# Kernel tuning notes

Measured on AMD Instinct MI355X. Metric: run time of the kernel, lower is better.

Reference implementation:

```python
import jax, jax.numpy as jnp
import numpy as np

D = 1024
H = 16
HD = D // H
SCALE = HD ** -0.5
LN_EPS = 1e-5


def _ln(x, g, b):
    m = x.mean(-1, keepdims=True)
    v = ((x - m) ** 2).mean(-1, keepdims=True)
    return (x - m) / jnp.sqrt(v + LN_EPS) * g + b


def _heads(x):
    B, S, _ = x.shape
    return x.reshape(B, S, H, HD).transpose(0, 2, 1, 3)  # [B,H,S,hd]


def setup_inputs() -> dict:
    key = jax.random.key(0)
    ks = jax.random.split(key, 32)
    it = iter(ks)

    def w():
        return jax.random.normal(next(it), (D, D), dtype=jnp.float32) * 0.02

    inp = {
        'q_text': jax.random.normal(next(it), (4, 512, D), dtype=jnp.float32),
        'q_image': jax.random.normal(next(it), (4, 576, D), dtype=jnp.float32),
        'k_text': jax.random.normal(next(it), (4, 512, D), dtype=jnp.float32),
        'k_image': jax.random.normal(next(it), (4, 576, D), dtype=jnp.float32),
        'Wq_text': w(), 'bq_text': jnp.zeros((D,), jnp.float32),
        'Wk_text': w(), 'bk_text': jnp.zeros((D,), jnp.float32),
        'Wv_text': w(), 'bv_text': jnp.zeros((D,), jnp.float32),
        'Wq_image': w(), 'bq_image': jnp.zeros((D,), jnp.float32),
        'Wk_image': w(), 'bk_image': jnp.zeros((D,), jnp.float32),
        'Wv_image': w(), 'bv_image': jnp.zeros((D,), jnp.float32),
        'ln_g_text': jnp.ones((D,), jnp.float32), 'ln_b_text': jnp.zeros((D,), jnp.float32),
        'ln_g_image': jnp.ones((D,), jnp.float32), 'ln_b_image': jnp.zeros((D,), jnp.float32),
        'Wo': w(), 'bo': jnp.zeros((D,), jnp.float32),
    }
    return inp


def reference(q_text, q_image, k_text, k_image,
              Wq_text, bq_text, Wk_text, bk_text, Wv_text, bv_text,
              Wq_image, bq_image, Wk_image, bk_image, Wv_image, bv_image,
              ln_g_text, ln_b_text, ln_g_image, ln_b_image, Wo, bo):
    # Normalize KV inputs per modality, project, split heads, concat along seq.
    kt = _ln(k_text, ln_g_text, ln_b_text)
    ki = _ln(k_image, ln_g_image, ln_b_image)
    K = jnp.concatenate([_heads(kt @ Wk_text.T + bk_text),
                         _heads(ki @ Wk_image.T + bk_image)], axis=2)  # [B,H,Skv,hd]
    # NOTE: torch module projects V from the `keys` tensors (values dict unused)
    V = jnp.concatenate([_heads(kt @ Wv_text.T + bv_text),
                         _heads(ki @ Wv_image.T + bv_image)], axis=2)

    def attend(q, g, b, Wq, bq):
        qn = _ln(q, g, b)
        Q = _heads(qn @ Wq.T + bq) * SCALE  # [B,H,Sq,hd]
        scores = jnp.einsum('bhqd,bhkd->bhqk', Q, K)
        w = jax.nn.softmax(scores.astype(jnp.float32), axis=-1).astype(q.dtype)
        o = jnp.einsum('bhqk,bhkd->bhqd', w, V)
        B, Sq = q.shape[0], q.shape[1]
        o = o.transpose(0, 2, 1, 3).reshape(B, Sq, D)
        return o @ Wo.T + bo, w

    out_t, w_t = attend(q_text, ln_g_text, ln_b_text, Wq_text, bq_text)
    out_i, w_i = attend(q_image, ln_g_image, ln_b_image, Wq_image, bq_image)
    return out_t, out_i, w_t, w_i
```

## Files before the change

kernel.cpp:

```cpp
#include <hip/hip_runtime.h>
#include <math.h>

#define DMODEL 1024
#define SKV 1088
#define SCALE 0.125f

typedef __attribute__((ext_vector_type(8))) short short8;
typedef __attribute__((ext_vector_type(4))) float floatx4;
typedef unsigned short ush;

__device__ __forceinline__ ush bf16_rne(float f) {
  unsigned u = __float_as_uint(f);
  u = (u + 0x7FFFu + ((u >> 16) & 1u)) >> 16;
  return (ush)u;
}
__device__ __forceinline__ float bf16_f32(ush h) {
  return __uint_as_float(((unsigned)h) << 16);
}

__global__ __launch_bounds__(256) void ln_split(const float* __restrict__ x,
                                                const float* __restrict__ g,
                                                const float* __restrict__ bta,
                                                ush* __restrict__ yh,
                                                ush* __restrict__ yl) {
  int row = blockIdx.x;
  const float4* xr = (const float4*)(x + (size_t)row * DMODEL);
  float4 v = xr[threadIdx.x];
  float s = v.x + v.y + v.z + v.w;
  float s2 = v.x * v.x + v.y * v.y + v.z * v.z + v.w * v.w;
  for (int off = 32; off > 0; off >>= 1) {
    s += __shfl_down(s, off, 64);
    s2 += __shfl_down(s2, off, 64);
  }
  __shared__ float ls[4], ls2[4];
  int wid = threadIdx.x >> 6;
  if ((threadIdx.x & 63) == 0) { ls[wid] = s; ls2[wid] = s2; }
  __syncthreads();
  float tot = ls[0] + ls[1] + ls[2] + ls[3];
  float tot2 = ls2[0] + ls2[1] + ls2[2] + ls2[3];
  float mean = tot * (1.0f / DMODEL);
  float var = tot2 * (1.0f / DMODEL) - mean * mean;
  float rstd = rsqrtf(var + 1e-5f);
  float4 gv = ((const float4*)g)[threadIdx.x];
  float4 bv = ((const float4*)bta)[threadIdx.x];
  float4 o;
  o.x = (v.x - mean) * rstd * gv.x + bv.x;
  o.y = (v.y - mean) * rstd * gv.y + bv.y;
  o.z = (v.z - mean) * rstd * gv.z + bv.z;
  o.w = (v.w - mean) * rstd * gv.w + bv.w;
  ushort4 hv, lv;
  hv.x = bf16_rne(o.x); lv.x = bf16_rne(o.x - bf16_f32(hv.x));
  hv.y = bf16_rne(o.y); lv.y = bf16_rne(o.y - bf16_f32(hv.y));
  hv.z = bf16_rne(o.z); lv.z = bf16_rne(o.z - bf16_f32(hv.z));
  hv.w = bf16_rne(o.w); lv.w = bf16_rne(o.w - bf16_f32(hv.w));
  ((ushort4*)(yh + (size_t)row * DMODEL))[threadIdx.x] = hv;
  ((ushort4*)(yl + (size_t)row * DMODEL))[threadIdx.x] = lv;
}

struct ConvJob { const float* src; ush* h; ush* l; int n4; };
struct ConvJobs { ConvJob j[4]; };

__global__ __launch_bounds__(256) void conv_split(ConvJobs jobs) {
  ConvJob jb = jobs.j[blockIdx.y];
  int i = blockIdx.x * 256 + threadIdx.x;
  if (i >= jb.n4) return;
  float4 v = ((const float4*)jb.src)[i];
  ushort4 hv, lv;
  hv.x = bf16_rne(v.x); lv.x = bf16_rne(v.x - bf16_f32(hv.x));
  hv.y = bf16_rne(v.y); lv.y = bf16_rne(v.y - bf16_f32(hv.y));
  hv.z = bf16_rne(v.z); lv.z = bf16_rne(v.z - bf16_f32(hv.z));
  hv.w = bf16_rne(v.w); lv.w = bf16_rne(v.w - bf16_f32(hv.w));
  ((ushort4*)jb.h)[i] = hv;
  ((ushort4*)jb.l)[i] = lv;
}

struct GemmSJob {
  const ush *Ah, *Al, *Wh, *Wl;
  const float* bias;
  float* C;
  ush* Cb;
  int M, Sin, Sout, seq_off;
  float scale;
};
struct GemmSJobs { GemmSJob j[4]; };

__device__ __forceinline__ int lds_slot(int m, int kc) {
  return m * 32 + ((kc ^ ((m >> 2) & 3)) << 3);
}

__global__ __launch_bounds__(256) void gemm_split(GemmSJobs jobs) {
  GemmSJob jb = jobs.j[blockIdx.z];
  const int m0 = blockIdx.y * 128;
  if (m0 >= jb.M) return;
  const int n0 = blockIdx.x * 128;

  __shared__ __align__(16) ush sAh[128 * 32];
  __shared__ __align__(16) ush sAl[128 * 32];
  __shared__ __align__(16) ush sWh[128 * 32];
  __shared__ __align__(16) ush sWl[128 * 32];

  const int tid = threadIdx.x;
  const int lane = tid & 63;
  const int wv = tid >> 6;
  const int wm = (wv & 1) * 64;
  const int wn = (wv >> 1) * 64;

  const int mS = tid >> 2;
  const int kcS = tid & 3;
  const int ls0 = lds_slot(mS, kcS);
  const int ls1 = lds_slot(mS + 64, kcS);
  const size_t aOff0 = (size_t)(m0 + mS) * DMODEL + kcS * 8;
  const size_t aOff1 = (size_t)(m0 + mS + 64) * DMODEL + kcS * 8;
  const size_t wOff0 = (size_t)(n0 + mS) * DMODEL + kcS * 8;
  const size_t wOff1 = (size_t)(n0 + mS + 64) * DMODEL + kcS * 8;

  const int fr = lane & 15, fc = lane >> 4;
  int offA[4], offB[4];
#pragma unroll
  for (int t = 0; t < 4; ++t) {
    offA[t] = lds_slot(wm + t * 16 + fr, fc);
    offB[t] = lds_slot(wn + t * 16 + fr, fc);
  }

  floatx4 acc[4][4];
#pragma unroll
  for (int mt = 0; mt < 4; ++mt)
#pragma unroll
    for (int nt = 0; nt < 4; ++nt) acc[mt][nt] = (floatx4){0.f, 0.f, 0.f, 0.f};

  uint4 rAh0 = *(const uint4*)(jb.Ah + aOff0);
  uint4 rAh1 = *(const uint4*)(jb.Ah + aOff1);
  uint4 rAl0 = *(const uint4*)(jb.Al + aOff0);
  uint4 rAl1 = *(const uint4*)(jb.Al + aOff1);
  uint4 rWh0 = *(const uint4*)(jb.Wh + wOff0);
  uint4 rWh1 = *(const uint4*)(jb.Wh + wOff1);
  uint4 rWl0 = *(const uint4*)(jb.Wl + wOff0);
  uint4 rWl1 = *(const uint4*)(jb.Wl + wOff1);

  for (int k0 = 0; k0 < DMODEL; k0 += 32) {
    __syncthreads();
    *(uint4*)(sAh + ls0) = rAh0;
    *(uint4*)(sAh + ls1) = rAh1;
    *(uint4*)(sAl + ls0) = rAl0;
    *(uint4*)(sAl + ls1) = rAl1;
    *(uint4*)(sWh + ls0) = rWh0;
    *(uint4*)(sWh + ls1) = rWh1;
    *(uint4*)(sWl + ls0) = rWl0;
    *(uint4*)(sWl + ls1) = rWl1;
    __syncthreads();
    if (k0 + 32 < DMODEL) {
      const int ko = k0 + 32;
      rAh0 = *(const uint4*)(jb.Ah + aOff0 + ko);
      rAh1 = *(const uint4*)(jb.Ah + aOff1 + ko);
      rAl0 = *(const uint4*)(jb.Al + aOff0 + ko);
      rAl1 = *(const uint4*)(jb.Al + aOff1 + ko);
      rWh0 = *(const uint4*)(jb.Wh + wOff0 + ko);
      rWh1 = *(const uint4*)(jb.Wh + wOff1 + ko);
      rWl0 = *(const uint4*)(jb.Wl + wOff0 + ko);
      rWl1 = *(const uint4*)(jb.Wl + wOff1 + ko);
    }
    short8 ah[4], al[4];
#pragma unroll
    for (int t = 0; t < 4; ++t) {
      ah[t] = *(const short8*)(sAh + offA[t]);
      al[t] = *(const short8*)(sAl + offA[t]);
    }
#pragma unroll
    for (int nt = 0; nt < 4; ++nt) {
      short8 bh = *(const short8*)(sWh + offB[nt]);
      short8 bl = *(const short8*)(sWl + offB[nt]);
#pragma unroll
      for (int mt = 0; mt < 4; ++mt) {
        acc[mt][nt] = __builtin_amdgcn_mfma_f32_16x16x32_bf16(ah[mt], bh, acc[mt][nt], 0, 0, 0);
        acc[mt][nt] = __builtin_amdgcn_mfma_f32_16x16x32_bf16(ah[mt], bl, acc[mt][nt], 0, 0, 0);
        acc[mt][nt] = __builtin_amdgcn_mfma_f32_16x16x32_bf16(al[mt], bh, acc[mt][nt], 0, 0, 0);
      }
    }
  }

  float bias_v[4];
#pragma unroll
  for (int nt = 0; nt < 4; ++nt) bias_v[nt] = jb.bias[n0 + wn + nt * 16 + fr];
  if (jb.Cb) {
#pragma unroll
    for (int mt = 0; mt < 4; ++mt) {
#pragma unroll
      for (int r = 0; r < 4; ++r) {
        int rowA = m0 + wm + mt * 16 + fc * 4 + r;
        int rowOut = (rowA / jb.Sin) * jb.Sout + jb.seq_off + (rowA % jb.Sin);
        ush* crow = jb.Cb + (size_t)rowOut * DMODEL + n0 + wn + fr;
#pragma unroll
        for (int nt = 0; nt < 4; ++nt)
          crow[nt * 16] = bf16_rne((acc[mt][nt][r] + bias_v[nt]) * jb.scale);
      }
    }
  } else {
#pragma unroll
    for (int mt = 0; mt < 4; ++mt) {
#pragma unroll
      for (int r = 0; r < 4; ++r) {
        int rowA = m0 + wm + mt * 16 + fc * 4 + r;
        int rowOut = (rowA / jb.Sin) * jb.Sout + jb.seq_off + (rowA % jb.Sin);
        float* crow = jb.C + (size_t)rowOut * DMODEL + n0 + wn + fr;
#pragma unroll
        for (int nt = 0; nt < 4; ++nt)
          crow[nt * 16] = (acc[mt][nt][r] + bias_v[nt]) * jb.scale;
      }
    }
  }
}

__global__ __launch_bounds__(256) void vtrans(const float* __restrict__ Vc, ush* __restrict__ Vt) {
  int k0 = blockIdx.x * 64;
  int bh = blockIdx.y;
  int b = bh >> 4, h = bh & 15;
  __shared__ ush T[64][72];
  int t = threadIdx.x;
  int c4 = (t & 15) * 4;
  int r = t >> 4;
#pragma unroll
  for (int i = 0; i < 4; ++i) {
    int kr = r + i * 16;
    float4 v = *(const float4*)(Vc + (size_t)(b * SKV + k0 + kr) * DMODEL + h * 64 + c4);
    T[c4 + 0][kr] = bf16_rne(v.x);
    T[c4 + 1][kr] = bf16_rne(v.y);
    T[c4 + 2][kr] = bf16_rne(v.z);
    T[c4 + 3][kr] = bf16_rne(v.w);
  }
  __syncthreads();
#pragma unroll
  for (int i = 0; i < 4; ++i) {
    int dr = r + i * 16;
    ushort4 o;
    o.x = T[dr][c4 + 0]; o.y = T[dr][c4 + 1]; o.z = T[dr][c4 + 2]; o.w = T[dr][c4 + 3];
    *(ushort4*)(Vt + ((size_t)bh * 64 + dr) * SKV + k0 + c4) = o;
  }
}

__global__ __launch_bounds__(256) void attn_mfma(
    const ush* __restrict__ Qt, const ush* __restrict__ Qi,
    const ush* __restrict__ Kbf, const ush* __restrict__ Vtp,
    float* __restrict__ Wt, float* __restrict__ Wi,
    ush* __restrict__ OtH, ush* __restrict__ OtL,
    ush* __restrict__ OiH, ush* __restrict__ OiL) {
  const int mod = blockIdx.z;
  const int Sq = mod ? 576 : 512;
  const int q0 = blockIdx.x * 32;
  if (q0 >= Sq) return;
  const int bh = blockIdx.y;
  const int b = bh >> 4, h = bh & 15;
  const ush* Q = mod ? Qi : Qt;
  float* Wout = mod ? Wi : Wt;
  ush* OH = mod ? OiH : OtH;
  ush* OL = mod ? OiL : OtL;

  const int tid = threadIdx.x;
  const int lane = tid & 63;
  const int wv = tid >> 6;
  const int qs = (wv & 1) * 16;
  const int half = wv >> 1;
  const int fr = lane & 15;
  const int fc = lane >> 4;

  __shared__ ush Psh[32][80];
  __shared__ float sm[2][2][16], sl[2][2][16];

  const ush* qrow = Q + (size_t)(b * Sq + q0 + qs + fr) * DMODEL + h * 64 + fc * 8;
  short8 qa0 = *(const short8*)qrow;
  short8 qa1 = *(const short8*)(qrow + 32);

  const ush* Kbase = Kbf + (size_t)b * SKV * DMODEL + h * 64 + fc * 8;
  const ush* Vbase = Vtp + (size_t)bh * 64 * SKV;

  float m[4], l[4];
#pragma unroll
  for (int r = 0; r < 4; ++r) { m[r] = -1e30f; l[r] = 0.f; }

  for (int k0 = 0; k0 < SKV; k0 += 64) {
    const ush* kr0 = Kbase + (size_t)(k0 + half * 32 + fr) * DMODEL;
    const ush* kr1 = kr0 + 16 * DMODEL;
    short8 b00 = *(const short8*)kr0;
    short8 b01 = *(const short8*)(kr0 + 32);
    short8 b10 = *(const short8*)kr1;
    short8 b11 = *(const short8*)(kr1 + 32);
    floatx4 s0 = (floatx4){0.f, 0.f, 0.f, 0.f};
    floatx4 s1 = (floatx4){0.f, 0.f, 0.f, 0.f};
    s0 = __builtin_amdgcn_mfma_f32_16x16x32_bf16(qa0, b00, s0, 0, 0, 0);
    s0 = __builtin_amdgcn_mfma_f32_16x16x32_bf16(qa1, b01, s0, 0, 0, 0);
    s1 = __builtin_amdgcn_mfma_f32_16x16x32_bf16(qa0, b10, s1, 0, 0, 0);
    s1 = __builtin_amdgcn_mfma_f32_16x16x32_bf16(qa1, b11, s1, 0, 0, 0);
#pragma unroll
    for (int r = 0; r < 4; ++r) {
      float mn = fmaxf(m[r], fmaxf(s0[r], s1[r]));
      l[r] = l[r] * __expf(m[r] - mn) + __expf(s0[r] - mn) + __expf(s1[r] - mn);
      m[r] = mn;
    }
  }
#pragma unroll
  for (int off = 1; off <= 8; off <<= 1) {
#pragma unroll
    for (int r = 0; r < 4; ++r) {
      float mo = __shfl_xor(m[r], off, 64);
      float lo = __shfl_xor(l[r], off, 64);
      float mn = fmaxf(m[r], mo);
      l[r] = l[r] * __expf(m[r] - mn) + lo * __expf(mo - mn);
      m[r] = mn;
    }
  }
  if (fr == 0) {
#pragma unroll
    for (int r = 0; r < 4; ++r) {
      sm[half][wv & 1][fc * 4 + r] = m[r];
      sl[half][wv & 1][fc * 4 + r] = l[r];
    }
  }
  __syncthreads();
  float mf[4], rl[4];
#pragma unroll
  for (int r = 0; r < 4; ++r) {
    int row = fc * 4 + r;
    float ma = sm[0][wv & 1][row], mb = sm[1][wv & 1][row];
    float la = sl[0][wv & 1][row], lb = sl[1][wv & 1][row];
    float mn = fmaxf(ma, mb);
    float lt = la * __expf(ma - mn) + lb * __expf(mb - mn);
    mf[r] = mn;
    rl[r] = 1.0f / lt;
  }

  floatx4 oacc0 = (floatx4){0.f, 0.f, 0.f, 0.f};
  floatx4 oacc1 = (floatx4){0.f, 0.f, 0.f, 0.f};

  for (int k0 = 0; k0 < SKV; k0 += 64) {
    const ush* kr0 = Kbase + (size_t)(k0 + half * 32 + fr) * DMODEL;
    const ush* kr1 = kr0 + 16 * DMODEL;
    short8 b00 = *(const short8*)kr0;
    short8 b01 = *(const short8*)(kr0 + 32);
    short8 b10 = *(const short8*)kr1;
    short8 b11 = *(const short8*)(kr1 + 32);
    floatx4 s0 = (floatx4){0.f, 0.f, 0.f, 0.f};
    floatx4 s1 = (floatx4){0.f, 0.f, 0.f, 0.f};
    s0 = __builtin_amdgcn_mfma_f32_16x16x32_bf16(qa0, b00, s0, 0, 0, 0);
    s0 = __builtin_amdgcn_mfma_f32_16x16x32_bf16(qa1, b01, s0, 0, 0, 0);
    s1 = __builtin_amdgcn_mfma_f32_16x16x32_bf16(qa0, b10, s1, 0, 0, 0);
    s1 = __builtin_amdgcn_mfma_f32_16x16x32_bf16(qa1, b11, s1, 0, 0, 0);
#pragma unroll
    for (int r = 0; r < 4; ++r) {
      float w0 = __expf(s0[r] - mf[r]) * rl[r];
      float w1 = __expf(s1[r] - mf[r]) * rl[r];
      int q = q0 + qs + fc * 4 + r;
      float* wr = Wout + ((size_t)bh * Sq + q) * SKV + k0 + half * 32 + fr;
      wr[0] = w0;
      wr[16] = w1;
      Psh[qs + fc * 4 + r][half * 32 + fr] = bf16_rne(w0);
      Psh[qs + fc * 4 + r][half * 32 + 16 + fr] = bf16_rne(w1);
    }
    __syncthreads();
    short8 pa0 = *(const short8*)&Psh[qs + fr][fc * 8];
    short8 pa1 = *(const short8*)&Psh[qs + fr][32 + fc * 8];
    const ush* v0 = Vbase + (size_t)(half * 32 + fr) * SKV + k0 + fc * 8;
    const ush* v1 = v0 + (size_t)16 * SKV;
    short8 vb00 = *(const short8*)v0;
    short8 vb01 = *(const short8*)(v0 + 32);
    short8 vb10 = *(const short8*)v1;
    short8 vb11 = *(const short8*)(v1 + 32);
    oacc0 = __builtin_amdgcn_mfma_f32_16x16x32_bf16(pa0, vb00, oacc0, 0, 0, 0);
    oacc0 = __builtin_amdgcn_mfma_f32_16x16x32_bf16(pa1, vb01, oacc0, 0, 0, 0);
    oacc1 = __builtin_amdgcn_mfma_f32_16x16x32_bf16(pa0, vb10, oacc1, 0, 0, 0);
    oacc1 = __builtin_amdgcn_mfma_f32_16x16x32_bf16(pa1, vb11, oacc1, 0, 0, 0);
    __syncthreads();
  }

#pragma unroll
  for (int r = 0; r < 4; ++r) {
    int q = q0 + qs + fc * 4 + r;
    size_t orow = (size_t)(b * Sq + q) * DMODEL + h * 64;
    float o0 = oacc0[r], o1 = oacc1[r];
    ush h0 = bf16_rne(o0);
    ush h1 = bf16_rne(o1);
    OH[orow + half * 32 + fr] = h0;
    OL[orow + half * 32 + fr] = bf16_rne(o0 - bf16_f32(h0));
    OH[orow + half * 32 + 16 + fr] = h1;
    OL[orow + half * 32 + 16 + fr] = bf16_rne(o1 - bf16_f32(h1));
  }
}

extern "C" void kernel_launch(void* const* d_in, const int* in_sizes, int n_in,
                              void* d_out, int out_size, void* d_ws, size_t ws_size,
                              hipStream_t stream) {
  const float* q_text = (const float*)d_in[0];
  const float* q_image = (const float*)d_in[1];
  const float* k_text = (const float*)d_in[2];
  const float* k_image = (const float*)d_in[3];
  const float* Wq_t = (const float*)d_in[4];
  const float* bq_t = (const float*)d_in[5];
  const float* Wk_t = (const float*)d_in[6];
  const float* bk_t = (const float*)d_in[7];
  const float* Wv_t = (const float*)d_in[8];
  const float* bv_t = (const float*)d_in[9];
  const float* Wq_i = (const float*)d_in[10];
  const float* bq_i = (const float*)d_in[11];
  const float* Wk_i = (const float*)d_in[12];
  const float* bk_i = (const float*)d_in[13];
  const float* Wv_i = (const float*)d_in[14];
  const float* bv_i = (const float*)d_in[15];
  const float* g_t = (const float*)d_in[16];
  const float* b_t = (const float*)d_in[17];
  const float* g_i = (const float*)d_in[18];
  const float* b_i = (const float*)d_in[19];
  const float* Wo = (const float*)d_in[20];
  const float* bo = (const float*)d_in[21];

  float* out = (float*)d_out;
  float* out_t = out;
  float* out_i = out + 2097152;
  float* w_t = out + 4456448;
  float* w_i = out + 40108032;

  char* W = (char*)d_ws;
  ush* Kbf = (ush*)(W + 0);
  ush* Qt_bf = (ush*)(W + 8912896);
  ush* Qi_bf = (ush*)(W + 13107200);
  float* Vc = (float*)(W + 17825792);
  ush* Vt = (ush*)(W + 35651584);
  char* R0 = W + 44564480;

  ush* knt_h = (ush*)(R0 + 0);
  ush* knt_l = (ush*)(R0 + 4194304);
  ush* kni_h = (ush*)(R0 + 8388608);
  ush* kni_l = (ush*)(R0 + 13107200);
  ush* wkt_h = (ush*)(R0 + 17825792);
  ush* wkt_l = (ush*)(R0 + 19922944);
  ush* wki_h = (ush*)(R0 + 22020096);
  ush* wki_l = (ush*)(R0 + 24117248);
  ush* wvt_h = (ush*)(R0 + 26214400);
  ush* wvt_l = (ush*)(R0 + 28311552);
  ush* wvi_h = (ush*)(R0 + 30408704);
  ush* wvi_l = (ush*)(R0 + 32505856);
  ush* qnt_h = (ush*)(R0 + 0);
  ush* qnt_l = (ush*)(R0 + 4194304);
  ush* qni_h = (ush*)(R0 + 8388608);
  ush* qni_l = (ush*)(R0 + 13107200);
  ush* wqt_h = (ush*)(R0 + 17825792);
  ush* wqt_l = (ush*)(R0 + 19922944);
  ush* wqi_h = (ush*)(R0 + 22020096);
  ush* wqi_l = (ush*)(R0 + 24117248);
  ush* ot_h = (ush*)(R0 + 0);
  ush* ot_l = (ush*)(R0 + 4194304);
  ush* oi_h = (ush*)(R0 + 8388608);
  ush* oi_l = (ush*)(R0 + 13107200);
  ush* wo_h = (ush*)(R0 + 17825792);
  ush* wo_l = (ush*)(R0 + 19922944);

  ln_split<<<2048, 256, 0, stream>>>(k_text, g_t, b_t, knt_h, knt_l);
  ln_split<<<2304, 256, 0, stream>>>(k_image, g_i, b_i, kni_h, kni_l);

  ConvJobs cw;
  cw.j[0] = {Wk_t, wkt_h, wkt_l, 262144};
  cw.j[1] = {Wk_i, wki_h, wki_l, 262144};
  cw.j[2] = {Wv_t, wvt_h, wvt_l, 262144};
  cw.j[3] = {Wv_i, wvi_h, wvi_l, 262144};
  conv_split<<<dim3(1024, 4), 256, 0, stream>>>(cw);

  GemmSJobs kv;
  kv.j[0] = {knt_h, knt_l, wkt_h, wkt_l, bk_t, nullptr, Kbf, 2048, 512, SKV, 0, 1.0f};
  kv.j[1] = {kni_h, kni_l, wki_h, wki_l, bk_i, nullptr, Kbf, 2304, 576, SKV, 512, 1.0f};
  kv.j[2] = {knt_h, knt_l, wvt_h, wvt_l, bv_t, Vc, nullptr, 2048, 512, SKV, 0, 1.0f};
  kv.j[3] = {kni_h, kni_l, wvi_h, wvi_l, bv_i, Vc, nullptr, 2304, 576, SKV, 512, 1.0f};
  gemm_split<<<dim3(8, 18, 4), 256, 0, stream>>>(kv);

  vtrans<<<dim3(17, 64), 256, 0, stream>>>(Vc, Vt);

  ln_split<<<2048, 256, 0, stream>>>(q_text, g_t, b_t, qnt_h, qnt_l);
  ln_split<<<2304, 256, 0, stream>>>(q_image, g_i, b_i, qni_h, qni_l);

  ConvJobs cq;
  cq.j[0] = {Wq_t, wqt_h, wqt_l, 262144};
  cq.j[1] = {Wq_i, wqi_h, wqi_l, 262144};
  cq.j[2] = cq.j[0];
  cq.j[3] = cq.j[0];
  conv_split<<<dim3(1024, 2), 256, 0, stream>>>(cq);

  GemmSJobs qj;
  qj.j[0] = {qnt_h, qnt_l, wqt_h, wqt_l, bq_t, nullptr, Qt_bf, 2048, 512, 512, 0, SCALE};
  qj.j[1] = {qni_h, qni_l, wqi_h, wqi_l, bq_i, nullptr, Qi_bf, 2304, 576, 576, 0, SCALE};
  qj.j[2] = qj.j[0];
  qj.j[3] = qj.j[0];
  gemm_split<<<dim3(8, 18, 2), 256, 0, stream>>>(qj);

  attn_mfma<<<dim3(18, 64, 2), 256, 0, stream>>>(Qt_bf, Qi_bf, Kbf, Vt,
                                                 w_t, w_i, ot_h, ot_l, oi_h, oi_l);

  ConvJobs cwo;
  cwo.j[0] = {Wo, wo_h, wo_l, 262144};
  cwo.j[1] = cwo.j[0];
  cwo.j[2] = cwo.j[0];
  cwo.j[3] = cwo.j[0];
  conv_split<<<dim3(1024, 1), 256, 0, stream>>>(cwo);

  GemmSJobs oj;
  oj.j[0] = {ot_h, ot_l, wo_h, wo_l, bo, out_t, nullptr, 2048, 512, 512, 0, 1.0f};
  oj.j[1] = {oi_h, oi_l, wo_h, wo_l, bo, out_i, nullptr, 2304, 576, 576, 0, 1.0f};
  oj.j[2] = oj.j[0];
  oj.j[3] = oj.j[0];
  gemm_split<<<dim3(8, 18, 2), 256, 0, stream>>>(oj);
}
```

Baseline: 774.8 us.

## Batch LN/convert/projection launches, use direct-to-LDS GEMM loads, restructure attention with LDS tiles

Merges the four layernorm launches into one, the K/V/Q weight conversions into one, and the K/V/Q projection GEMMs into a single six-job launch. V is now written as bf16 instead of fp32, which halves the transpose traffic. The GEMM stages tiles through global_load_lds when available, but it drops the register prefetch and so loses load/compute overlap. Attention now uses 64-query blocks that share K/V tiles in swizzled LDS across four waves, trading extra barriers for less redundant global traffic.

```diff
diff --git a/kernel.cpp b/kernel.cpp
--- a/kernel.cpp
+++ b/kernel.cpp
@@ -18,13 +18,26 @@
   return __uint_as_float(((unsigned)h) << 16);
 }
 
-__global__ __launch_bounds__(256) void ln_split(const float* __restrict__ x,
-                                                const float* __restrict__ g,
-                                                const float* __restrict__ bta,
-                                                ush* __restrict__ yh,
-                                                ush* __restrict__ yl) {
+#if __has_builtin(__builtin_amdgcn_global_load_lds)
+#define HAS_GLL 1
+__device__ __forceinline__ void gll16(const ush* g, ush* l) {
+  __builtin_amdgcn_global_load_lds(
+      (const __attribute__((address_space(1))) unsigned int*)g,
+      (__attribute__((address_space(3))) unsigned int*)(unsigned int)(size_t)l,
+      16, 0, 0);
+}
+#else
+#define HAS_GLL 0
+#endif
+
+struct LnJob { const float* x; const float* g; const float* b; ush* yh; ush* yl; int rows; };
+struct LnJobs { LnJob j[4]; };
+
+__global__ __launch_bounds__(256) void ln_all(LnJobs jobs) {
+  LnJob jb = jobs.j[blockIdx.y];
   int row = blockIdx.x;
-  const float4* xr = (const float4*)(x + (size_t)row * DMODEL);
+  if (row >= jb.rows) return;
+  const float4* xr = (const float4*)(jb.x + (size_t)row * DMODEL);
   float4 v = xr[threadIdx.x];
   float s = v.x + v.y + v.z + v.w;
   float s2 = v.x * v.x + v.y * v.y + v.z * v.z + v.w * v.w;
@@ -41,8 +54,8 @@
   float mean = tot * (1.0f / DMODEL);
   float var = tot2 * (1.0f / DMODEL) - mean * mean;
   float rstd = rsqrtf(var + 1e-5f);
-  float4 gv = ((const float4*)g)[threadIdx.x];
-  float4 bv = ((const float4*)bta)[threadIdx.x];
+  float4 gv = ((const float4*)jb.g)[threadIdx.x];
+  float4 bv = ((const float4*)jb.b)[threadIdx.x];
   float4 o;
   o.x = (v.x - mean) * rstd * gv.x + bv.x;
   o.y = (v.y - mean) * rstd * gv.y + bv.y;
@@ -53,12 +66,12 @@
   hv.y = bf16_rne(o.y); lv.y = bf16_rne(o.y - bf16_f32(hv.y));
   hv.z = bf16_rne(o.z); lv.z = bf16_rne(o.z - bf16_f32(hv.z));
   hv.w = bf16_rne(o.w); lv.w = bf16_rne(o.w - bf16_f32(hv.w));
-  ((ushort4*)(yh + (size_t)row * DMODEL))[threadIdx.x] = hv;
-  ((ushort4*)(yl + (size_t)row * DMODEL))[threadIdx.x] = lv;
+  ((ushort4*)(jb.yh + (size_t)row * DMODEL))[threadIdx.x] = hv;
+  ((ushort4*)(jb.yl + (size_t)row * DMODEL))[threadIdx.x] = lv;
 }
 
 struct ConvJob { const float* src; ush* h; ush* l; int n4; };
-struct ConvJobs { ConvJob j[4]; };
+struct ConvJobs { ConvJob j[6]; };
 
 __global__ __launch_bounds__(256) void conv_split(ConvJobs jobs) {
   ConvJob jb = jobs.j[blockIdx.y];
@@ -82,7 +95,7 @@
   int M, Sin, Sout, seq_off;
   float scale;
 };
-struct GemmSJobs { GemmSJob j[4]; };
+struct GemmSJobs { GemmSJob j[6]; };
 
 __device__ __forceinline__ int lds_slot(int m, int kc) {
   return m * 32 + ((kc ^ ((m >> 2) & 3)) << 3);
@@ -94,10 +107,10 @@
   if (m0 >= jb.M) return;
   const int n0 = blockIdx.x * 128;
 
-  __shared__ __align__(16) ush sAh[128 * 32];
-  __shared__ __align__(16) ush sAl[128 * 32];
-  __shared__ __align__(16) ush sWh[128 * 32];
-  __shared__ __align__(16) ush sWl[128 * 32];
+  __shared__ __align__(16) ush sAh[4096];
+  __shared__ __align__(16) ush sAl[4096];
+  __shared__ __align__(16) ush sWh[4096];
+  __shared__ __align__(16) ush sWl[4096];
 
   const int tid = threadIdx.x;
   const int lane = tid & 63;
@@ -105,14 +118,14 @@
   const int wm = (wv & 1) * 64;
   const int wn = (wv >> 1) * 64;
 
-  const int mS = tid >> 2;
-  const int kcS = tid & 3;
-  const int ls0 = lds_slot(mS, kcS);
-  const int ls1 = lds_slot(mS + 64, kcS);
-  const size_t aOff0 = (size_t)(m0 + mS) * DMODEL + kcS * 8;
-  const size_t aOff1 = (size_t)(m0 + mS + 64) * DMODEL + kcS * 8;
-  const size_t wOff0 = (size_t)(n0 + mS) * DMODEL + kcS * 8;
-  const size_t wOff1 = (size_t)(n0 + mS + 64) * DMODEL + kcS * 8;
+  const int rowS = tid >> 2;
+  const int kcS = (tid & 3) ^ ((rowS >> 2) & 3);
+  const size_t aOff0 = (size_t)(m0 + rowS) * DMODEL + kcS * 8;
+  const size_t aOff1 = aOff0 + (size_t)64 * DMODEL;
+  const size_t wOff0 = (size_t)(n0 + rowS) * DMODEL + kcS * 8;
+  const size_t wOff1 = wOff0 + (size_t)64 * DMODEL;
+  const int lq0 = tid * 8;
+  const int lq1 = 2048 + tid * 8;
 
   const int fr = lane & 15, fc = lane >> 4;
   int offA[4], offB[4];
@@ -128,37 +141,34 @@
 #pragma unroll
     for (int nt = 0; nt < 4; ++nt) acc[mt][nt] = (floatx4){0.f, 0.f, 0.f, 0.f};
 
-  uint4 rAh0 = *(const uint4*)(jb.Ah + aOff0);
-  uint4 rAh1 = *(const uint4*)(jb.Ah + aOff1);
-  uint4 rAl0 = *(const uint4*)(jb.Al + aOff0);
-  uint4 rAl1 = *(const uint4*)(jb.Al + aOff1);
-  uint4 rWh0 = *(const uint4*)(jb.Wh + wOff0);
-  uint4 rWh1 = *(const uint4*)(jb.Wh + wOff1);
-  uint4 rWl0 = *(const uint4*)(jb.Wl + wOff0);
-  uint4 rWl1 = *(const uint4*)(jb.Wl + wOff1);
-
   for (int k0 = 0; k0 < DMODEL; k0 += 32) {
     __syncthreads();
-    *(uint4*)(sAh + ls0) = rAh0;
-    *(uint4*)(sAh + ls1) = rAh1;
-    *(uint4*)(sAl + ls0) = rAl0;
-    *(uint4*)(sAl + ls1) = rAl1;
-    *(uint4*)(sWh + ls0) = rWh0;
-    *(uint4*)(sWh + ls1) = rWh1;
-    *(uint4*)(sWl + ls0) = rWl0;
-    *(uint4*)(sWl + ls1) = rWl1;
+#if HAS_GLL
+    gll16(jb.Ah + aOff0 + k0, sAh + lq0);
+    gll16(jb.Ah + aOff1 + k0, sAh + lq1);
+    gll16(jb.Al + aOff0 + k0, sAl + lq0);
+    gll16(jb.Al + aOff1 + k0, sAl + lq1);
+    gll16(jb.Wh + wOff0 + k0, sWh + lq0);
+    gll16(jb.Wh + wOff1 + k0, sWh + lq1);
+    gll16(jb.Wl + wOff0 + k0, sWl + lq0);
+    gll16(jb.Wl + wOff1 + k0, sWl + lq1);
+#else
+    {
+      uint4 a0 = *(const uint4*)(jb.Ah + aOff0 + k0);
+      uint4 a1 = *(const uint4*)(jb.Ah + aOff1 + k0);
+      uint4 b0 = *(const uint4*)(jb.Al + aOff0 + k0);
+      uint4 b1 = *(const uint4*)(jb.Al + aOff1 + k0);
+      uint4 c0 = *(const uint4*)(jb.Wh + wOff0 + k0);
+      uint4 c1 = *(const uint4*)(jb.Wh + wOff1 + k0);
+      uint4 d0 = *(const uint4*)(jb.Wl + wOff0 + k0);
+      uint4 d1 = *(const uint4*)(jb.Wl + wOff1 + k0);
+      *(uint4*)(sAh + lq0) = a0; *(uint4*)(sAh + lq1) = a1;
+      *(uint4*)(sAl + lq0) = b0; *(uint4*)(sAl + lq1) = b1;
+      *(uint4*)(sWh + lq0) = c0; *(uint4*)(sWh + lq1) = c1;
+      *(uint4*)(sWl + lq0) = d0; *(uint4*)(sWl + lq1) = d1;
+    }
+#endif
     __syncthreads();
-    if (k0 + 32 < DMODEL) {
-      const int ko = k0 + 32;
-      rAh0 = *(const uint4*)(jb.Ah + aOff0 + ko);
-      rAh1 = *(const uint4*)(jb.Ah + aOff1 + ko);
-      rAl0 = *(const uint4*)(jb.Al + aOff0 + ko);
-      rAl1 = *(const uint4*)(jb.Al + aOff1 + ko);
-      rWh0 = *(const uint4*)(jb.Wh + wOff0 + ko);
-      rWh1 = *(const uint4*)(jb.Wh + wOff1 + ko);
-      rWl0 = *(const uint4*)(jb.Wl + wOff0 + ko);
-      rWl1 = *(const uint4*)(jb.Wl + wOff1 + ko);
-    }
     short8 ah[4], al[4];
 #pragma unroll
     for (int t = 0; t < 4; ++t) {
@@ -210,7 +220,7 @@
   }
 }
 
-__global__ __launch_bounds__(256) void vtrans(const float* __restrict__ Vc, ush* __restrict__ Vt) {
+__global__ __launch_bounds__(256) void vtrans(const ush* __restrict__ Vbf, ush* __restrict__ Vt) {
   int k0 = blockIdx.x * 64;
   int bh = blockIdx.y;
   int b = bh >> 4, h = bh & 15;
@@ -221,11 +231,11 @@
 #pragma unroll
   for (int i = 0; i < 4; ++i) {
     int kr = r + i * 16;
-    float4 v = *(const float4*)(Vc + (size_t)(b * SKV + k0 + kr) * DMODEL + h * 64 + c4);
-    T[c4 + 0][kr] = bf16_rne(v.x);
-    T[c4 + 1][kr] = bf16_rne(v.y);
-    T[c4 + 2][kr] = bf16_rne(v.z);
-    T[c4 + 3][kr] = bf16_rne(v.w);
+    ushort4 v = *(const ushort4*)(Vbf + (size_t)(b * SKV + k0 + kr) * DMODEL + h * 64 + c4);
+    T[c4 + 0][kr] = v.x;
+    T[c4 + 1][kr] = v.y;
+    T[c4 + 2][kr] = v.z;
+    T[c4 + 3][kr] = v.w;
   }
   __syncthreads();
 #pragma unroll
@@ -238,61 +248,86 @@
 }
 
 __global__ __launch_bounds__(256) void attn_mfma(
-    const ush* __restrict__ Qt, const ush* __restrict__ Qi,
+    const ush* __restrict__ Qtb, const ush* __restrict__ Qib,
     const ush* __restrict__ Kbf, const ush* __restrict__ Vtp,
     float* __restrict__ Wt, float* __restrict__ Wi,
     ush* __restrict__ OtH, ush* __restrict__ OtL,
     ush* __restrict__ OiH, ush* __restrict__ OiL) {
   const int mod = blockIdx.z;
   const int Sq = mod ? 576 : 512;
-  const int q0 = blockIdx.x * 32;
+  const int q0 = blockIdx.x * 64;
   if (q0 >= Sq) return;
   const int bh = blockIdx.y;
   const int b = bh >> 4, h = bh & 15;
-  const ush* Q = mod ? Qi : Qt;
+  const ush* Q = mod ? Qib : Qtb;
   float* Wout = mod ? Wi : Wt;
   ush* OH = mod ? OiH : OtH;
   ush* OL = mod ? OiL : OtL;
 
+  __shared__ __align__(16) ush sK[64 * 64];
+  __shared__ __align__(16) ush sV[64 * 64];
+  __shared__ __align__(16) ush sP[4][16 * 64];
+
   const int tid = threadIdx.x;
   const int lane = tid & 63;
   const int wv = tid >> 6;
-  const int qs = (wv & 1) * 16;
-  const int half = wv >> 1;
   const int fr = lane & 15;
   const int fc = lane >> 4;
 
-  __shared__ ush Psh[32][80];
-  __shared__ float sm[2][2][16], sl[2][2][16];
-
-  const ush* qrow = Q + (size_t)(b * Sq + q0 + qs + fr) * DMODEL + h * 64 + fc * 8;
+  const int srow = tid >> 2;
+  const int sch = (tid & 3) * 2;
+  const int ssl = sch ^ (srow & 7);
+  ush* skw0 = sK + srow * 64 + ssl * 8;
+  ush* skw1 = sK + srow * 64 + (ssl ^ 1) * 8;
+  ush* svw0 = sV + srow * 64 + ssl * 8;
+  ush* svw1 = sV + srow * 64 + (ssl ^ 1) * 8;
+  const ush* Kg = Kbf + (size_t)(b * SKV + srow) * DMODEL + h * 64 + sch * 8;
+  const ush* Vg = Vtp + ((size_t)bh * 64 + srow) * SKV + sch * 8;
+
+  const ush* qrow = Q + (size_t)(b * Sq + q0 + wv * 16 + fr) * DMODEL + h * 64 + fc * 8;
   short8 qa0 = *(const short8*)qrow;
   short8 qa1 = *(const short8*)(qrow + 32);
 
-  const ush* Kbase = Kbf + (size_t)b * SKV * DMODEL + h * 64 + fc * 8;
-  const ush* Vbase = Vtp + (size_t)bh * 64 * SKV;
+  const int sw = fr & 7;
+  int kOffL[4], kOffH[4];
+#pragma unroll
+  for (int j = 0; j < 4; ++j) {
+    int base = (j * 16 + fr) * 64;
+    kOffL[j] = base + (fc ^ sw) * 8;
+    kOffH[j] = base + ((fc + 4) ^ sw) * 8;
+  }
+  const int pOffL = fr * 64 + (fc ^ sw) * 8;
+  const int pOffH = fr * 64 + ((fc + 4) ^ sw) * 8;
 
   float m[4], l[4];
 #pragma unroll
-  for (int r = 0; r < 4; ++r) { m[r] = -1e30f; l[r] = 0.f; }
-
-  for (int k0 = 0; k0 < SKV; k0 += 64) {
-    const ush* kr0 = Kbase + (size_t)(k0 + half * 32 + fr) * DMODEL;
-    const ush* kr1 = kr0 + 16 * DMODEL;
-    short8 b00 = *(const short8*)kr0;
-    short8 b01 = *(const short8*)(kr0 + 32);
-    short8 b10 = *(const short8*)kr1;
-    short8 b11 = *(const short8*)(kr1 + 32);
-    floatx4 s0 = (floatx4){0.f, 0.f, 0.f, 0.f};
-    floatx4 s1 = (floatx4){0.f, 0.f, 0.f, 0.f};
-    s0 = __builtin_amdgcn_mfma_f32_16x16x32_bf16(qa0, b00, s0, 0, 0, 0);
-    s0 = __builtin_amdgcn_mfma_f32_16x16x32_bf16(qa1, b01, s0, 0, 0, 0);
-    s1 = __builtin_amdgcn_mfma_f32_16x16x32_bf16(qa0, b10, s1, 0, 0, 0);
-    s1 = __builtin_amdgcn_mfma_f32_16x16x32_bf16(qa1, b11, s1, 0, 0, 0);
+  for (int r = 0; r < 4; ++r) { m[r] = -3e38f; l[r] = 0.f; }
+
+  for (int kt = 0; kt < 17; ++kt) {
+    __syncthreads();
+    {
+      const ush* kp = Kg + (size_t)(kt * 64) * DMODEL;
+      uint4 x = *(const uint4*)kp;
+      uint4 y = *(const uint4*)(kp + 8);
+      *(uint4*)skw0 = x;
+      *(uint4*)skw1 = y;
+    }
+    __syncthreads();
+    floatx4 s[4];
+#pragma unroll
+    for (int j = 0; j < 4; ++j) {
+      short8 b0 = *(const short8*)(sK + kOffL[j]);
+      short8 b1 = *(const short8*)(sK + kOffH[j]);
+      floatx4 z = (floatx4){0.f, 0.f, 0.f, 0.f};
+      z = __builtin_amdgcn_mfma_f32_16x16x32_bf16(qa0, b0, z, 0, 0, 0);
+      s[j] = __builtin_amdgcn_mfma_f32_16x16x32_bf16(qa1, b1, z, 0, 0, 0);
+    }
 #pragma unroll
     for (int r = 0; r < 4; ++r) {
-      float mn = fmaxf(m[r], fmaxf(s0[r], s1[r]));
-      l[r] = l[r] * __expf(m[r] - mn) + __expf(s0[r] - mn) + __expf(s1[r] - mn);
+      float mx = fmaxf(fmaxf(s[0][r], s[1][r]), fmaxf(s[2][r], s[3][r]));
+      float mn = fmaxf(m[r], mx);
+      l[r] = l[r] * __expf(m[r] - mn) + __expf(s[0][r] - mn) + __expf(s[1][r] - mn) +
+             __expf(s[2][r] - mn) + __expf(s[3][r] - mn);
       m[r] = mn;
     }
   }
@@ -307,80 +342,74 @@
       m[r] = mn;
     }
   }
-  if (fr == 0) {
+  float rl[4];
+#pragma unroll
+  for (int r = 0; r < 4; ++r) rl[r] = 1.0f / l[r];
+
+  floatx4 oacc[4];
+#pragma unroll
+  for (int j = 0; j < 4; ++j) oacc[j] = (floatx4){0.f, 0.f, 0.f, 0.f};
+
+  float* wbase = Wout + ((size_t)bh * Sq + q0 + wv * 16) * SKV;
+
+  for (int kt = 0; kt < 17; ++kt) {
+    const int k0 = kt * 64;
+    __syncthreads();
+    {
+      const ush* kp = Kg + (size_t)k0 * DMODEL;
+      uint4 x = *(const uint4*)kp;
+      uint4 y = *(const uint4*)(kp + 8);
+      const ush* vp = Vg + k0;
+      uint4 vx = *(const uint4*)vp;
+      uint4 vy = *(const uint4*)(vp + 8);
+      *(uint4*)skw0 = x;
+      *(uint4*)skw1 = y;
+      *(uint4*)svw0 = vx;
+      *(uint4*)svw1 = vy;
+    }
+    __syncthreads();
+    floatx4 s[4];
+#pragma unroll
+    for (int j = 0; j < 4; ++j) {
+      short8 b0 = *(const short8*)(sK + kOffL[j]);
+      short8 b1 = *(const short8*)(sK + kOffH[j]);
+      floatx4 z = (floatx4){0.f, 0.f, 0.f, 0.f};
+      z = __builtin_amdgcn_mfma_f32_16x16x32_bf16(qa0, b0, z, 0, 0, 0);
+      s[j] = __builtin_amdgcn_mfma_f32_16x16x32_bf16(qa1, b1, s[j] = z, 0, 0, 0);
+    }
+#pragma unroll
+    for (int j = 0; j < 4; ++j) {
+#pragma unroll
+      for (int r = 0; r < 4; ++r) {
+        float w = __expf(s[j][r] - m[r]) * rl[r];
+        wbase[(size_t)(fc * 4 + r) * SKV + k0 + j * 16 + fr] = w;
+        int row = fc * 4 + r;
+        int chunk = j * 2 + (fr >> 3);
+        sP[wv][row * 64 + ((chunk ^ (row & 7)) * 8) + (fr & 7)] = bf16_rne(w);
+      }
+    }
+    short8 pa0 = *(const short8*)(sP[wv] + pOffL);
+    short8 pa1 = *(const short8*)(sP[wv] + pOffH);
+#pragma unroll
+    for (int j = 0; j < 4; ++j) {
+      short8 v0 = *(const short8*)(sV + kOffL[j]);
+      short8 v1 = *(const short8*)(sV + kOffH[j]);
+      oacc[j] = __builtin_amdgcn_mfma_f32_16x16x32_bf16(pa0, v0, oacc[j], 0, 0, 0);
+      oacc[j] = __builtin_amdgcn_mfma_f32_16x16x32_bf16(pa1, v1, oacc[j], 0, 0, 0);
+    }
+  }
+
+#pragma unroll
+  for (int j = 0; j < 4; ++j) {
 #pragma unroll
     for (int r = 0; r < 4; ++r) {
-      sm[half][wv & 1][fc * 4 + r] = m[r];
-      sl[half][wv & 1][fc * 4 + r] = l[r];
-    }
-  }
-  __syncthreads();
-  float mf[4], rl[4];
-#pragma unroll
-  for (int r = 0; r < 4; ++r) {
-    int row = fc * 4 + r;
-    float ma = sm[0][wv & 1][row], mb = sm[1][wv & 1][row];
-    float la = sl[0][wv & 1][row], lb = sl[1][wv & 1][row];
-    float mn = fmaxf(ma, mb);
-    float lt = la * __expf(ma - mn) + lb * __expf(mb - mn);
-    mf[r] = mn;
-    rl[r] = 1.0f / lt;
-  }
-
-  floatx4 oacc0 = (floatx4){0.f, 0.f, 0.f, 0.f};
-  floatx4 oacc1 = (floatx4){0.f, 0.f, 0.f, 0.f};
-
-  for (int k0 = 0; k0 < SKV; k0 += 64) {
-    const ush* kr0 = Kbase + (size_t)(k0 + half * 32 + fr) * DMODEL;
-    const ush* kr1 = kr0 + 16 * DMODEL;
-    short8 b00 = *(const short8*)kr0;
-    short8 b01 = *(const short8*)(kr0 + 32);
-    short8 b10 = *(const short8*)kr1;
-    short8 b11 = *(const short8*)(kr1 + 32);
-    floatx4 s0 = (floatx4){0.f, 0.f, 0.f, 0.f};
-    floatx4 s1 = (floatx4){0.f, 0.f, 0.f, 0.f};
-    s0 = __builtin_amdgcn_mfma_f32_16x16x32_bf16(qa0, b00, s0, 0, 0, 0);
-    s0 = __builtin_amdgcn_mfma_f32_16x16x32_bf16(qa1, b01, s0, 0, 0, 0);
-    s1 = __builtin_amdgcn_mfma_f32_16x16x32_bf16(qa0, b10, s1, 0, 0, 0);
-    s1 = __builtin_amdgcn_mfma_f32_16x16x32_bf16(qa1, b11, s1, 0, 0, 0);
-#pragma unroll
-    for (int r = 0; r < 4; ++r) {
-      float w0 = __expf(s0[r] - mf[r]) * rl[r];
-      float w1 = __expf(s1[r] - mf[r]) * rl[r];
-      int q = q0 + qs + fc * 4 + r;
-      float* wr = Wout + ((size_t)bh * Sq + q) * SKV + k0 + half * 32 + fr;
-      wr[0] = w0;
-      wr[16] = w1;
-      Psh[qs + fc * 4 + r][half * 32 + fr] = bf16_rne(w0);
-      Psh[qs + fc * 4 + r][half * 32 + 16 + fr] = bf16_rne(w1);
-    }
-    __syncthreads();
-    short8 pa0 = *(const short8*)&Psh[qs + fr][fc * 8];
-    short8 pa1 = *(const short8*)&Psh[qs + fr][32 + fc * 8];
-    const ush* v0 = Vbase + (size_t)(half * 32 + fr) * SKV + k0 + fc * 8;
-    const ush* v1 = v0 + (size_t)16 * SKV;
-    short8 vb00 = *(const short8*)v0;
-    short8 vb01 = *(const short8*)(v0 + 32);
-    short8 vb10 = *(const short8*)v1;
-    short8 vb11 = *(const short8*)(v1 + 32);
-    oacc0 = __builtin_amdgcn_mfma_f32_16x16x32_bf16(pa0, vb00, oacc0, 0, 0, 0);
-    oacc0 = __builtin_amdgcn_mfma_f32_16x16x32_bf16(pa1, vb01, oacc0, 0, 0, 0);
-    oacc1 = __builtin_amdgcn_mfma_f32_16x16x32_bf16(pa0, vb10, oacc1, 0, 0, 0);
-    oacc1 = __builtin_amdgcn_mfma_f32_16x16x32_bf16(pa1, vb11, oacc1, 0, 0, 0);
-    __syncthreads();
-  }
-
-#pragma unroll
-  for (int r = 0; r < 4; ++r) {
-    int q = q0 + qs + fc * 4 + r;
-    size_t orow = (size_t)(b * Sq + q) * DMODEL + h * 64;
-    float o0 = oacc0[r], o1 = oacc1[r];
-    ush h0 = bf16_rne(o0);
-    ush h1 = bf16_rne(o1);
-    OH[orow + half * 32 + fr] = h0;
-    OL[orow + half * 32 + fr] = bf16_rne(o0 - bf16_f32(h0));
-    OH[orow + half * 32 + 16 + fr] = h1;
-    OL[orow + half * 32 + 16 + fr] = bf16_rne(o1 - bf16_f32(h1));
+      int q = q0 + wv * 16 + fc * 4 + r;
+      size_t oidx = (size_t)(b * Sq + q) * DMODEL + h * 64 + j * 16 + fr;
+      float o = oacc[j][r];
+      ush hh = bf16_rne(o);
+      OH[oidx] = hh;
+      OL[oidx] = bf16_rne(o - bf16_f32(hh));
+    }
   }
 }
 
@@ -418,89 +447,76 @@
 
   char* W = (char*)d_ws;
   ush* Kbf = (ush*)(W + 0);
-  ush* Qt_bf = (ush*)(W + 8912896);
-  ush* Qi_bf = (ush*)(W + 13107200);
-  float* Vc = (float*)(W + 17825792);
-  ush* Vt = (ush*)(W + 35651584);
-  char* R0 = W + 44564480;
-
-  ush* knt_h = (ush*)(R0 + 0);
-  ush* knt_l = (ush*)(R0 + 4194304);
-  ush* kni_h = (ush*)(R0 + 8388608);
-  ush* kni_l = (ush*)(R0 + 13107200);
-  ush* wkt_h = (ush*)(R0 + 17825792);
-  ush* wkt_l = (ush*)(R0 + 19922944);
-  ush* wki_h = (ush*)(R0 + 22020096);
-  ush* wki_l = (ush*)(R0 + 24117248);
-  ush* wvt_h = (ush*)(R0 + 26214400);
-  ush* wvt_l = (ush*)(R0 + 28311552);
-  ush* wvi_h = (ush*)(R0 + 30408704);
-  ush* wvi_l = (ush*)(R0 + 32505856);
-  ush* qnt_h = (ush*)(R0 + 0);
-  ush* qnt_l = (ush*)(R0 + 4194304);
-  ush* qni_h = (ush*)(R0 + 8388608);
-  ush* qni_l = (ush*)(R0 + 13107200);
-  ush* wqt_h = (ush*)(R0 + 17825792);
-  ush* wqt_l = (ush*)(R0 + 19922944);
-  ush* wqi_h = (ush*)(R0 + 22020096);
-  ush* wqi_l = (ush*)(R0 + 24117248);
-  ush* ot_h = (ush*)(R0 + 0);
-  ush* ot_l = (ush*)(R0 + 4194304);
-  ush* oi_h = (ush*)(R0 + 8388608);
-  ush* oi_l = (ush*)(R0 + 13107200);
-  ush* wo_h = (ush*)(R0 + 17825792);
-  ush* wo_l = (ush*)(R0 + 19922944);
-
-  ln_split<<<2048, 256, 0, stream>>>(k_text, g_t, b_t, knt_h, knt_l);
-  ln_split<<<2304, 256, 0, stream>>>(k_image, g_i, b_i, kni_h, kni_l);
+  ush* Vbf = (ush*)(W + 8912896);
+  ush* Qt_bf = (ush*)(W + 17825792);
+  ush* Qi_bf = (ush*)(W + 22020096);
+  ush* knt_h = (ush*)(W + 26738688);
+  ush* knt_l = (ush*)(W + 30932992);
+  ush* kni_h = (ush*)(W + 35127296);
+  ush* kni_l = (ush*)(W + 39845888);
+  ush* qnt_h = (ush*)(W + 44564480);
+  ush* qnt_l = (ush*)(W + 48758784);
+  ush* qni_h = (ush*)(W + 52953088);
+  ush* qni_l = (ush*)(W + 57671680);
+  ush* wkt_h = (ush*)(W + 62390272);
+  ush* wkt_l = (ush*)(W + 64487424);
+  ush* wki_h = (ush*)(W + 66584576);
+  ush* wki_l = (ush*)(W + 68681728);
+  ush* wvt_h = (ush*)(W + 70778880);
+  ush* wvt_l = (ush*)(W + 72876032);
+  ush* wvi_h = (ush*)(W + 74973184);
+  ush* wvi_l = (ush*)(W + 77070336);
+  ush* wqt_h = (ush*)(W + 79167488);
+  ush* wqt_l = (ush*)(W + 81264640);
+  ush* wqi_h = (ush*)(W + 83361792);
+  ush* wqi_l = (ush*)(W + 85458944);
+  ush* Vt = (ush*)(W + 44564480);
+  ush* wo_h = (ush*)(W + 53477376);
+  ush* wo_l = (ush*)(W + 55574528);
+  ush* ot_h = knt_h;
+  ush* ot_l = knt_l;
+  ush* oi_h = kni_h;
+  ush* oi_l = kni_l;
+
+  LnJobs lj;
+  lj.j[0] = {k_text, g_t, b_t, knt_h, knt_l, 2048};
+  lj.j[1] = {k_image, g_i, b_i, kni_h, kni_l, 2304};
+  lj.j[2] = {q_text, g_t, b_t, qnt_h, qnt_l, 2048};
+  lj.j[3] = {q_image, g_i, b_i, qni_h, qni_l, 2304};
+  ln_all<<<dim3(2304, 4), 256, 0, stream>>>(lj);
 
   ConvJobs cw;
   cw.j[0] = {Wk_t, wkt_h, wkt_l, 262144};
   cw.j[1] = {Wk_i, wki_h, wki_l, 262144};
   cw.j[2] = {Wv_t, wvt_h, wvt_l, 262144};
   cw.j[3] = {Wv_i, wvi_h, wvi_l, 262144};
-  conv_split<<<dim3(1024, 4), 256, 0, stream>>>(cw);
-
-  GemmSJobs kv;
-  kv.j[0] = {knt_h, knt_l, wkt_h, wkt_l, bk_t, nullptr, Kbf, 2048, 512, SKV, 0, 1.0f};
-  kv.j[1] = {kni_h, kni_l, wki_h, wki_l, bk_i, nullptr, Kbf, 2304, 576, SKV, 512, 1.0f};
-  kv.j[2] = {knt_h, knt_l, wvt_h, wvt_l, bv_t, Vc, nullptr, 2048, 512, SKV, 0, 1.0f};
-  kv.j[3] = {kni_h, kni_l, wvi_h, wvi_l, bv_i, Vc, nullptr, 2304, 576, SKV, 512, 1.0f};
-  gemm_split<<<dim3(8, 18, 4), 256, 0, stream>>>(kv);
-
-  vtrans<<<dim3(17, 64), 256, 0, stream>>>(Vc, Vt);
-
-  ln_split<<<2048, 256, 0, stream>>>(q_text, g_t, b_t, qnt_h, qnt_l);
-  ln_split<<<2304, 256, 0, stream>>>(q_image, g_i, b_i, qni_h, qni_l);
-
-  ConvJobs cq;
-  cq.j[0] = {Wq_t, wqt_h, wqt_l, 262144};
-  cq.j[1] = {Wq_i, wqi_h, wqi_l, 262144};
-  cq.j[2] = cq.j[0];
-  cq.j[3] = cq.j[0];
-  conv_split<<<dim3(1024, 2), 256, 0, stream>>>(cq);
-
-  GemmSJobs qj;
-  qj.j[0] = {qnt_h, qnt_l, wqt_h, wqt_l, bq_t, nullptr, Qt_bf, 2048, 512, 512, 0, SCALE};
-  qj.j[1] = {qni_h, qni_l, wqi_h, wqi_l, bq_i, nullptr, Qi_bf, 2304, 576, 576, 0, SCALE};
-  qj.j[2] = qj.j[0];
-  qj.j[3] = qj.j[0];
-  gemm_split<<<dim3(8, 18, 2), 256, 0, stream>>>(qj);
-
-  attn_mfma<<<dim3(18, 64, 2), 256, 0, stream>>>(Qt_bf, Qi_bf, Kbf, Vt,
-                                                 w_t, w_i, ot_h, ot_l, oi_h, oi_l);
+  cw.j[4] = {Wq_t, wqt_h, wqt_l, 262144};
+  cw.j[5] = {Wq_i, wqi_h, wqi_l, 262144};
+  conv_split<<<dim3(1024, 6), 256, 0, stream>>>(cw);
+
+  GemmSJobs pj;
+  pj.j[0] = {knt_h, knt_l, wkt_h, wkt_l, bk_t, nullptr, Kbf, 2048, 512, SKV, 0, 1.0f};
+  pj.j[1] = {kni_h, kni_l, wki_h, wki_l, bk_i, nullptr, Kbf, 2304, 576, SKV, 512, 1.0f};
+  pj.j[2] = {knt_h, knt_l, wvt_h, wvt_l, bv_t, nullptr, Vbf, 2048, 512, SKV, 0, 1.0f};
+  pj.j[3] = {kni_h, kni_l, wvi_h, wvi_l, bv_i, nullptr, Vbf, 2304, 576, SKV, 512, 1.0f};
+  pj.j[4] = {qnt_h, qnt_l, wqt_h, wqt_l, bq_t, nullptr, Qt_bf, 2048, 512, 512, 0, SCALE};
+  pj.j[5] = {qni_h, qni_l, wqi_h, wqi_l, bq_i, nullptr, Qi_bf, 2304, 576, 576, 0, SCALE};
+  gemm_split<<<dim3(8, 18, 6), 256, 0, stream>>>(pj);
+
+  vtrans<<<dim3(17, 64), 256, 0, stream>>>(Vbf, Vt);
 
   ConvJobs cwo;
   cwo.j[0] = {Wo, wo_h, wo_l, 262144};
-  cwo.j[1] = cwo.j[0];
-  cwo.j[2] = cwo.j[0];
-  cwo.j[3] = cwo.j[0];
+  cwo.j[1] = cwo.j[0]; cwo.j[2] = cwo.j[0];
+  cwo.j[3] = cwo.j[0]; cwo.j[4] = cwo.j[0]; cwo.j[5] = cwo.j[0];
   conv_split<<<dim3(1024, 1), 256, 0, stream>>>(cwo);
+
+  attn_mfma<<<dim3(9, 64, 2), 256, 0, stream>>>(Qt_bf, Qi_bf, Kbf, Vt,
+                                                w_t, w_i, ot_h, ot_l, oi_h, oi_l);
 
   GemmSJobs oj;
   oj.j[0] = {ot_h, ot_l, wo_h, wo_l, bo, out_t, nullptr, 2048, 512, 512, 0, 1.0f};
   oj.j[1] = {oi_h, oi_l, wo_h, wo_l, bo, out_i, nullptr, 2304, 576, 576, 0, 1.0f};
-  oj.j[2] = oj.j[0];
-  oj.j[3] = oj.j[0];
+  oj.j[2] = oj.j[0]; oj.j[3] = oj.j[0]; oj.j[4] = oj.j[0]; oj.j[5] = oj.j[0];
   gemm_split<<<dim3(8, 18, 2), 256, 0, stream>>>(oj);
 }
```

Measured after the change: 643.8 us. 1.2x faster.
